# Performance work log

Measured on AMD Instinct MI355X. Metric: run time of the kernel, lower is better.

## Reference

```python
import jax, jax.numpy as jnp
import numpy as np

D_MODEL = 1024
N_HEADS = 16
D_K = D_MODEL // N_HEADS
D_FF = 4096
B, S = 2, 2048
EPS = 1e-5


def setup_inputs() -> dict:
    key = jax.random.key(0)
    ks = jax.random.split(key, 16)
    sc = 0.02
    inp = {
        'x': jax.random.normal(ks[0], (B, S, D_MODEL), dtype=jnp.float32),
        'mask': jnp.ones((B, 1, 1, S), dtype=jnp.int32),
        'Wq': jax.random.normal(ks[1], (D_MODEL, D_MODEL), dtype=jnp.float32) * sc,
        'bq': jnp.zeros((D_MODEL,), dtype=jnp.float32),
        'Wk': jax.random.normal(ks[2], (D_MODEL, D_MODEL), dtype=jnp.float32) * sc,
        'bk': jnp.zeros((D_MODEL,), dtype=jnp.float32),
        'Wv': jax.random.normal(ks[3], (D_MODEL, D_MODEL), dtype=jnp.float32) * sc,
        'bv': jnp.zeros((D_MODEL,), dtype=jnp.float32),
        'Wo': jax.random.normal(ks[4], (D_MODEL, D_MODEL), dtype=jnp.float32) * sc,
        'bo': jnp.zeros((D_MODEL,), dtype=jnp.float32),
        'W1': jax.random.normal(ks[5], (D_MODEL, D_FF), dtype=jnp.float32) * sc,
        'b1': jnp.zeros((D_FF,), dtype=jnp.float32),
        'W2': jax.random.normal(ks[6], (D_FF, D_MODEL), dtype=jnp.float32) * sc,
        'b2': jnp.zeros((D_MODEL,), dtype=jnp.float32),
        'g1': jnp.ones((D_MODEL,), dtype=jnp.float32),
        'be1': jnp.zeros((D_MODEL,), dtype=jnp.float32),
        'g2': jnp.ones((D_MODEL,), dtype=jnp.float32),
        'be2': jnp.zeros((D_MODEL,), dtype=jnp.float32),
    }
    return inp


def _layernorm(x, g, b):
    mu = jnp.mean(x, axis=-1, keepdims=True)
    var = jnp.mean(jnp.square(x - mu), axis=-1, keepdims=True)
    return (x - mu) * jax.lax.rsqrt(var + EPS) * g + b


def _split_heads(x):
    b, s, _ = x.shape
    return x.reshape(b, s, N_HEADS, D_K).transpose(0, 2, 1, 3)  # [B,H,S,Dk]


def reference(x, mask, Wq, bq, Wk, bk, Wv, bv, Wo, bo, W1, b1, W2, b2, g1, be1, g2, be2):
    Q = _split_heads(x @ Wq + bq)
    K = _split_heads(x @ Wk + bk)
    V = _split_heads(x @ Wv + bv)
    scores = jnp.einsum('bhqd,bhkd->bhqk', Q, K) / jnp.sqrt(jnp.float32(D_K))
    scores = jnp.where(mask == 0, -jnp.inf, scores)
    attn = jax.nn.softmax(scores, axis=-1)
    ctx = jnp.einsum('bhqk,bhkd->bhqd', attn, V)
    ctx = ctx.transpose(0, 2, 1, 3).reshape(x.shape[0], x.shape[1], D_MODEL)
    attn_out = ctx @ Wo + bo
    h = _layernorm(x + attn_out, g1, be1)
    ff = jax.nn.relu(h @ W1 + b1) @ W2 + b2
    return _layernorm(h + ff, g2, be2)
```

## Files before the change

kernel.cpp:

```cpp
#include <hip/hip_runtime.h>
#include <hip/hip_bf16.h>

#define D_MODELC 1024
#define D_FFC    4096
#define N_HEADSC 16
#define BATCHC   2
#define SEQC     2048
#define M_TOK    (BATCHC*SEQC)

typedef __attribute__((ext_vector_type(4)))  float f32x4;
typedef __attribute__((ext_vector_type(16))) float f32x16;
typedef __attribute__((ext_vector_type(8)))  short s16x8;
using bf16_t = __hip_bfloat16;

static __device__ __forceinline__ unsigned short f2bf_u16(float f) {
  bf16_t h = __float2bfloat16(f);
  return __builtin_bit_cast(unsigned short, h);
}

static __device__ __forceinline__ unsigned int cvt_pk_bf16(float lo, float hi2) {
  unsigned int r;
  asm("v_cvt_pk_bf16_f32 %0, %1, %2" : "=v"(r) : "v"(lo), "v"(hi2));
  return r;
}

#define ASYNC_COPY16(dst_lds, src_g) \
  __builtin_amdgcn_global_load_lds((const __attribute__((address_space(1))) void*)(src_g), \
                                   (__attribute__((address_space(3))) void*)(dst_lds), 16, 0, 0)

__global__ __launch_bounds__(256) void k_transpose_f32_bf16(
    const float* __restrict__ in, bf16_t* __restrict__ out, int R, int C) {
  __shared__ float tile[32][33];
  int tx = threadIdx.x & 31, ty = threadIdx.x >> 5;
  int c0 = blockIdx.x * 32, r0 = blockIdx.y * 32;
#pragma unroll
  for (int i = 0; i < 4; ++i)
    tile[ty + i * 8][tx] = in[(size_t)(r0 + ty + i * 8) * C + c0 + tx];
  __syncthreads();
#pragma unroll
  for (int i = 0; i < 4; ++i)
    out[(size_t)(c0 + ty + i * 8) * R + r0 + tx] = __float2bfloat16(tile[tx][ty + i * 8]);
}

__global__ __launch_bounds__(256) void k_f32_to_bf16(
    const float* __restrict__ in, bf16_t* __restrict__ out, int n4) {
  int i = blockIdx.x * 256 + threadIdx.x;
  if (i < n4) {
    float4 v = ((const float4*)in)[i];
    short4 o;
    o.x = (short)f2bf_u16(v.x);
    o.y = (short)f2bf_u16(v.y);
    o.z = (short)f2bf_u16(v.z);
    o.w = (short)f2bf_u16(v.w);
    ((short4*)out)[i] = o;
  }
}

__global__ __launch_bounds__(256) void k_pack_bias(
    const float* __restrict__ bq, const float* __restrict__ bk,
    const float* __restrict__ bv, float* __restrict__ out) {
  int i = blockIdx.x * 256 + threadIdx.x;
  float v = (i < 1024) ? bq[i] : (i < 2048) ? bk[i - 1024] : bv[i - 2048];
  out[i] = v;
}

#define GBK 64

__global__ __launch_bounds__(256, 2) void k_gemm(
    const bf16_t* __restrict__ A, const bf16_t* __restrict__ BT,
    const float* __restrict__ bias,
    float* __restrict__ p0, float* __restrict__ p1,
    void* __restrict__ Cout, int M, int N, int K,
    int lda, int ldb, int ldc, int mode, int nsplit) {
  __shared__ __align__(16) bf16_t Asm[128 * GBK];
  __shared__ __align__(16) bf16_t Bsm[128 * GBK];

  const int nbn = N / 128;
  const int nwg = gridDim.x;
  const int cpx = nwg >> 3;
  int wg = (blockIdx.x & 7) * cpx + (blockIdx.x >> 3);
  int kslice = 0;
  if (nsplit == 2) { kslice = wg & 1; wg >>= 1; }
  const int mb = wg / nbn, nb = wg % nbn;
  const int row0 = mb * 128, col0 = nb * 128;
  A  += (size_t)kslice * K;
  BT += (size_t)kslice * K;

  const int tid = threadIdx.x;
  const int w = tid >> 6, lane = tid & 63;
  const int lr = lane & 15, lg = lane >> 4;
  const int wr = w >> 1, wc = w & 1;
  const int wbase = tid & 192;

  f32x4 acc[4][4];
#pragma unroll
  for (int m = 0; m < 4; ++m)
#pragma unroll
    for (int n = 0; n < 4; ++n) acc[m][n] = (f32x4){0.f, 0.f, 0.f, 0.f};

  for (int k0 = 0; k0 < K; k0 += GBK) {
    __syncthreads();
#pragma unroll
    for (int i = 0; i < 4; ++i) {
      int c = i * 256 + tid;
      int row = c >> 3;
      int sg = (c & 7) ^ (row & 7);
      ASYNC_COPY16(Asm + (size_t)(i * 256 + wbase) * 8,
                   A + (size_t)(row0 + row) * lda + k0 + sg * 8);
    }
#pragma unroll
    for (int i = 0; i < 4; ++i) {
      int c = i * 256 + tid;
      int row = c >> 3;
      int sg = (c & 7) ^ (row & 7);
      ASYNC_COPY16(Bsm + (size_t)(i * 256 + wbase) * 8,
                   BT + (size_t)(col0 + row) * ldb + k0 + sg * 8);
    }
    __syncthreads();
#pragma unroll
    for (int kst = 0; kst < 2; ++kst) {
      const int sl = ((kst * 4 + lg) ^ (lr & 7)) * 8;
      s16x8 af[4], bfr[4];
#pragma unroll
      for (int m = 0; m < 4; ++m)
        af[m] = *(const s16x8*)(Asm + (size_t)(wr * 64 + m * 16 + lr) * GBK + sl);
#pragma unroll
      for (int n = 0; n < 4; ++n)
        bfr[n] = *(const s16x8*)(Bsm + (size_t)(wc * 64 + n * 16 + lr) * GBK + sl);
#pragma unroll
      for (int m = 0; m < 4; ++m)
#pragma unroll
        for (int n = 0; n < 4; ++n)
          acc[m][n] = __builtin_amdgcn_mfma_f32_16x16x32_bf16(af[m], bfr[n], acc[m][n], 0, 0, 0);
    }
  }

  float* outf = (kslice == 0) ? p0 : p1;
  bf16_t* outh = (bf16_t*)Cout;
#pragma unroll
  for (int m = 0; m < 4; ++m) {
    int grow = row0 + wr * 64 + m * 16 + lg * 4;
#pragma unroll
    for (int n = 0; n < 4; ++n) {
      int gcol = col0 + wc * 64 + n * 16 + lr;
      float bv = (mode == 4) ? 0.f : bias[gcol];
      float cs = (mode == 3 && gcol < 1024) ? 0.18033688f : 1.f;
#pragma unroll
      for (int r = 0; r < 4; ++r) {
        float v = (acc[m][n][r] + bv) * cs;
        size_t idx = (size_t)(grow + r) * ldc + gcol;
        if (mode == 4) {
          outf[idx] = v;
        } else {
          if (mode == 1) v = fmaxf(v, 0.f);
          outh[idx] = __float2bfloat16(v);
        }
      }
    }
  }
}

__global__ __launch_bounds__(256, 2) void k_attn(
    const bf16_t* __restrict__ qkv, const int* __restrict__ mask,
    bf16_t* __restrict__ ctx) {
  const int bid = blockIdx.x;
  const int qt = bid & 15;
  const int h  = (bid >> 4) & 15;
  const int b  = bid >> 8;
  const int tid = threadIdx.x;
  const int w = tid >> 6, lane = tid & 63;
  const int l31 = lane & 31, hi = lane >> 5;

  __shared__ __align__(16) bf16_t Kl[2][64][64];
  __shared__ __align__(16) bf16_t VT[2][64][72];
  __shared__ __align__(16) float  mskf[2][64];

  const int tokb = b * SEQC;
  const int q0 = qt * 128 + w * 32;

  s16x8 qfrag[4];
  {
    const bf16_t* qp = qkv + (size_t)(tokb + q0 + l31) * 3072 + h * 64 + hi * 8;
#pragma unroll
    for (int s = 0; s < 4; ++s) qfrag[s] = *(const s16x8*)(qp + s * 16);
  }

  char* klc = (char*)&Kl[0][0][0];
  char* vtc = (char*)&VT[0][0][0];

  s16x8 vr[2];
  float mreg = 1.f;

#define STAGE_K(buf, kb)                                                              \
  {                                                                                   \
    _Pragma("unroll")                                                                 \
    for (int ii = 0; ii < 2; ++ii) {                                                  \
      int chunk = w * 2 + ii;                                                         \
      int row = chunk * 8 + (lane >> 3);                                              \
      int seg = (lane & 7) ^ (row & 7);                                               \
      const bf16_t* src = qkv + (size_t)(tokb + (kb) + row) * 3072 + 1024 + h * 64 + seg * 8; \
      ASYNC_COPY16(&Kl[buf][chunk * 8][0], src);                                      \
    }                                                                                 \
  }

#define LOAD_V(kb)                                                                    \
  {                                                                                   \
    _Pragma("unroll")                                                                 \
    for (int i = 0; i < 2; ++i) {                                                     \
      int c = tid + i * 256;                                                          \
      int key = c & 63, d0 = (c >> 6) * 8;                                            \
      vr[i] = *(const s16x8*)(qkv + (size_t)(tokb + (kb) + key) * 3072 + 2048 + h * 64 + d0); \
    }                                                                                 \
  }

#define WRITE_V(buf)                                                                  \
  {                                                                                   \
    _Pragma("unroll")                                                                 \
    for (int i = 0; i < 2; ++i) {                                                     \
      int c = tid + i * 256;                                                          \
      int key = c & 63, d0 = (c >> 6) * 8;                                            \
      const bf16_t* e = (const bf16_t*)&vr[i];                                        \
      _Pragma("unroll")                                                               \
      for (int j = 0; j < 8; ++j) {                                                   \
        int d = d0 + j;                                                               \
        *(bf16_t*)(vtc + (buf) * 9216 + d * 144 + (key >> 3) * 16 + (key & 7) * 2) = e[j]; \
      }                                                                               \
    }                                                                                 \
  }

  STAGE_K(0, 0)
  LOAD_V(0)
  if (tid < 64) mreg = mask[tokb + tid] ? 1.f : 0.f;
  WRITE_V(0)
  if (tid < 64) mskf[0][tid] = mreg;

  f32x16 o[2];
#pragma unroll
  for (int d = 0; d < 2; ++d)
#pragma unroll
    for (int i = 0; i < 16; ++i) o[d][i] = 0.f;
  float psum = 0.f;

  __syncthreads();

  for (int kt = 0; kt < SEQC / 64; ++kt) {
    const int kb = kt * 64;
    const int cur = kt & 1, nxt = cur ^ 1;
    const bool more = (kt < SEQC / 64 - 1);

    if (more) {
      STAGE_K(nxt, kb + 64)
      LOAD_V(kb + 64)
      if (tid < 64) mreg = mask[tokb + kb + 64 + tid] ? 1.f : 0.f;
    }

    f32x16 st[2];
#pragma unroll
    for (int kk = 0; kk < 2; ++kk)
#pragma unroll
      for (int i = 0; i < 16; ++i) st[kk][i] = 0.f;
#pragma unroll
    for (int step = 0; step < 4; ++step) {
#pragma unroll
      for (int kb2 = 0; kb2 < 2; ++kb2) {
        int key = kb2 * 32 + l31;
        int seg = (2 * step + hi) ^ (lane & 7);
        s16x8 kf = *(const s16x8*)(klc + cur * 8192 + key * 128 + seg * 16);
        st[kb2] = __builtin_amdgcn_mfma_f32_32x32x16_bf16(kf, qfrag[step], st[kb2], 0, 0, 0);
      }
    }

    s16x8 pf[4];
#pragma unroll
    for (int kb2 = 0; kb2 < 2; ++kb2) {
      float pa[16];
#pragma unroll
      for (int g = 0; g < 4; ++g) {
        f32x4 mm = *(const f32x4*)((char*)&mskf[cur][0] + (kb2 * 128 + g * 32 + hi * 16));
#pragma unroll
        for (int rr = 0; rr < 4; ++rr) {
          float e = __builtin_exp2f(st[kb2][g * 4 + rr]) * mm[rr];
          pa[g * 4 + rr] = e;
          psum += e;
        }
      }
      unsigned int wv[8];
#pragma unroll
      for (int u = 0; u < 8; ++u) wv[u] = cvt_pk_bf16(pa[2 * u], pa[2 * u + 1]);
      unsigned int x1 = hi ? wv[0] : wv[2]; x1 = (unsigned int)__shfl_xor((int)x1, 32);
      unsigned int x2 = hi ? wv[1] : wv[3]; x2 = (unsigned int)__shfl_xor((int)x2, 32);
      unsigned int x3 = hi ? wv[4] : wv[6]; x3 = (unsigned int)__shfl_xor((int)x3, 32);
      unsigned int x4 = hi ? wv[5] : wv[7]; x4 = (unsigned int)__shfl_xor((int)x4, 32);
      unsigned int f0[4], f1[4];
      f0[0] = hi ? x1 : wv[0];  f0[1] = hi ? x2 : wv[1];
      f0[2] = hi ? wv[2] : x1;  f0[3] = hi ? wv[3] : x2;
      f1[0] = hi ? x3 : wv[4];  f1[1] = hi ? x4 : wv[5];
      f1[2] = hi ? wv[6] : x3;  f1[3] = hi ? wv[7] : x4;
      pf[kb2 * 2 + 0] = __builtin_bit_cast(s16x8, *(ulong2*)f0);
      pf[kb2 * 2 + 1] = __builtin_bit_cast(s16x8, *(ulong2*)f1);
    }

#pragma unroll
    for (int ks = 0; ks < 4; ++ks) {
#pragma unroll
      for (int dblk = 0; dblk < 2; ++dblk) {
        int d = dblk * 32 + l31;
        s16x8 vf = *(const s16x8*)(vtc + cur * 9216 + d * 144 + (2 * ks + hi) * 16);
        o[dblk] = __builtin_amdgcn_mfma_f32_32x32x16_bf16(pf[ks], vf, o[dblk], 0, 0, 0);
      }
    }

    if (more) {
      WRITE_V(nxt)
      if (tid < 64) mskf[nxt][tid] = mreg;
    }

    __syncthreads();
  }

  psum += __shfl_xor(psum, 32);
  float rs[16];
#pragma unroll
  for (int r = 0; r < 16; ++r) {
    int qq = (r & 3) + 8 * (r >> 2) + 4 * hi;
    rs[r] = __shfl(psum, qq);
  }
#pragma unroll
  for (int dblk = 0; dblk < 2; ++dblk)
#pragma unroll
    for (int r = 0; r < 16; ++r) {
      int qq = (r & 3) + 8 * (r >> 2) + 4 * hi;
      int tok = tokb + q0 + qq;
      ctx[(size_t)tok * 1024 + h * 64 + dblk * 32 + l31] = __float2bfloat16(o[dblk][r] / rs[r]);
    }
#undef STAGE_K
#undef LOAD_V
#undef WRITE_V
}

__global__ __launch_bounds__(256) void k_ln_res2(
    const float* __restrict__ p0, const float* __restrict__ p1,
    const float* __restrict__ res, const float* __restrict__ bias,
    const float* __restrict__ g, const float* __restrict__ be,
    float* __restrict__ outf, bf16_t* __restrict__ outh) {
  const int row = blockIdx.x, tid = threadIdx.x;
  const size_t base = (size_t)row * D_MODELC;
  const float4 a  = ((const float4*)(p0 + base))[tid];
  const float4 bq = ((const float4*)(p1 + base))[tid];
  const float4 c  = ((const float4*)(res + base))[tid];
  const float4 bi = ((const float4*)bias)[tid];
  float4 v;
  v.x = a.x + bq.x + c.x + bi.x;
  v.y = a.y + bq.y + c.y + bi.y;
  v.z = a.z + bq.z + c.z + bi.z;
  v.w = a.w + bq.w + c.w + bi.w;
  float s1 = v.x + v.y + v.z + v.w;
  float s2 = v.x * v.x + v.y * v.y + v.z * v.z + v.w * v.w;
#pragma unroll
  for (int mm = 1; mm < 64; mm <<= 1) {
    s1 += __shfl_xor(s1, mm);
    s2 += __shfl_xor(s2, mm);
  }
  __shared__ float sa[4], sb[4];
  const int wv = tid >> 6;
  if ((tid & 63) == 0) { sa[wv] = s1; sb[wv] = s2; }
  __syncthreads();
  s1 = sa[0] + sa[1] + sa[2] + sa[3];
  s2 = sb[0] + sb[1] + sb[2] + sb[3];
  const float mu = s1 * (1.f / D_MODELC);
  const float var = s2 * (1.f / D_MODELC) - mu * mu;
  const float rsq = rsqrtf(var + 1e-5f);
  const float4 gg = ((const float4*)g)[tid];
  const float4 bb = ((const float4*)be)[tid];
  float4 oo;
  oo.x = (v.x - mu) * rsq * gg.x + bb.x;
  oo.y = (v.y - mu) * rsq * gg.y + bb.y;
  oo.z = (v.z - mu) * rsq * gg.z + bb.z;
  oo.w = (v.w - mu) * rsq * gg.w + bb.w;
  ((float4*)(outf + base))[tid] = oo;
  if (outh) {
    short4 ob;
    ob.x = (short)f2bf_u16(oo.x);
    ob.y = (short)f2bf_u16(oo.y);
    ob.z = (short)f2bf_u16(oo.z);
    ob.w = (short)f2bf_u16(oo.w);
    ((short4*)(outh + base))[tid] = ob;
  }
}

extern "C" void kernel_launch(void* const* d_in, const int* in_sizes, int n_in,
                              void* d_out, int out_size, void* d_ws, size_t ws_size,
                              hipStream_t stream) {
  (void)in_sizes; (void)n_in; (void)out_size; (void)ws_size;
  const float* x   = (const float*)d_in[0];
  const int* mask  = (const int*)d_in[1];
  const float* Wq  = (const float*)d_in[2];
  const float* bq  = (const float*)d_in[3];
  const float* Wk  = (const float*)d_in[4];
  const float* bk  = (const float*)d_in[5];
  const float* Wv  = (const float*)d_in[6];
  const float* bv  = (const float*)d_in[7];
  const float* Wo  = (const float*)d_in[8];
  const float* bo  = (const float*)d_in[9];
  const float* W1  = (const float*)d_in[10];
  const float* b1  = (const float*)d_in[11];
  const float* W2  = (const float*)d_in[12];
  const float* b2  = (const float*)d_in[13];
  const float* g1  = (const float*)d_in[14];
  const float* be1 = (const float*)d_in[15];
  const float* g2  = (const float*)d_in[16];
  const float* be2 = (const float*)d_in[17];

  char* ws = (char*)d_ws;
  const size_t D = D_MODELC, F = D_FFC, M = M_TOK;
  const size_t SZ_X16  = M * D * 2;
  const size_t SZ_QKV  = M * 3 * D * 2;
  bf16_t* x16   = (bf16_t*)ws;
  bf16_t* ff1   = (bf16_t*)ws;
  bf16_t* qkvb  = (bf16_t*)(ws + SZ_X16);
  size_t off = SZ_X16 + SZ_QKV;
  bf16_t* ctx   = (bf16_t*)(ws + off); off += M * D * 2;
  bf16_t* wqkvT = (bf16_t*)(ws + off); off += 3 * D * D * 2;
  bf16_t* woT   = (bf16_t*)(ws + off); off += D * D * 2;
  bf16_t* w1T   = (bf16_t*)(ws + off); off += D * F * 2;
  bf16_t* w2T   = (bf16_t*)(ws + off); off += D * F * 2;
  float*  partA = (float*)(ws + off);  off += M * D * 4;
  float*  hbuf  = (float*)(ws + off);  off += M * D * 4;
  bf16_t* h16   = (bf16_t*)(ws + off); off += M * D * 2;
  float*  partB = (float*)(ws + off);  off += M * D * 4;
  float*  bqkv  = (float*)(ws + off);  off += 3 * D * 4;

  k_transpose_f32_bf16<<<dim3(32, 32), 256, 0, stream>>>(Wq, wqkvT, 1024, 1024);
  k_transpose_f32_bf16<<<dim3(32, 32), 256, 0, stream>>>(Wk, wqkvT + 1024 * 1024, 1024, 1024);
  k_transpose_f32_bf16<<<dim3(32, 32), 256, 0, stream>>>(Wv, wqkvT + 2 * 1024 * 1024, 1024, 1024);
  k_transpose_f32_bf16<<<dim3(32, 32), 256, 0, stream>>>(Wo, woT, 1024, 1024);
  k_transpose_f32_bf16<<<dim3(128, 32), 256, 0, stream>>>(W1, w1T, 1024, 4096);
  k_transpose_f32_bf16<<<dim3(32, 128), 256, 0, stream>>>(W2, w2T, 4096, 1024);
  k_f32_to_bf16<<<4096, 256, 0, stream>>>(x, x16, (int)(M * D / 4));
  k_pack_bias<<<12, 256, 0, stream>>>(bq, bk, bv, bqkv);

  k_gemm<<<768, 256, 0, stream>>>(x16, wqkvT, bqkv, nullptr, nullptr, qkvb,
                                  4096, 3072, 1024, 1024, 1024, 3072, 3, 1);

  k_attn<<<BATCHC * N_HEADSC * (SEQC / 128), 256, 0, stream>>>(qkvb, mask, ctx);

  k_gemm<<<512, 256, 0, stream>>>(ctx, woT, nullptr, partA, partB, nullptr,
                                  4096, 1024, 512, 1024, 1024, 1024, 4, 2);
  k_ln_res2<<<4096, 256, 0, stream>>>(partA, partB, x, bo, g1, be1, hbuf, h16);

  k_gemm<<<1024, 256, 0, stream>>>(h16, w1T, b1, nullptr, nullptr, ff1,
                                   4096, 4096, 1024, 1024, 1024, 4096, 1, 1);
  k_gemm<<<512, 256, 0, stream>>>(ff1, w2T, nullptr, partA, partB, nullptr,
                                  4096, 1024, 2048, 4096, 4096, 1024, 4, 2);
  k_ln_res2<<<4096, 256, 0, stream>>>(partA, partB, hbuf, b2, g2, be2, (float*)d_out, nullptr);
}
```

Measured before the change: 275.2 us.

## Stage V via async LDS copy and transpose-read it, add all-valid mask fast path

Replaces the register-load-then-scalar-transposed-write of V tiles with direct async global-to-LDS copies in a permuted layout. V fragments are then read with the ds_read_b64_tr_b16 transpose-load instruction. The cross-half P fragment exchange now uses v_permlane32_swap instead of shfl_xor plus selects. A per-tile all-valid mask flag is computed with a ballot so the exp loop can skip the mask multiply. The intent is to cut LDS store traffic, VGPR pressure and VALU work in the attention loop, at the cost of relying on gfx950-specific instructions and a hand-placed waitcnt.

```diff
diff --git a/kernel.cpp b/kernel.cpp
--- a/kernel.cpp
+++ b/kernel.cpp
@@ -23,6 +23,8 @@
   asm("v_cvt_pk_bf16_f32 %0, %1, %2" : "=v"(r) : "v"(lo), "v"(hi2));
   return r;
 }
+
+#define PSWAP(a, b) asm volatile("v_permlane32_swap_b32 %0, %1" : "+v"(a), "+v"(b))
 
 #define ASYNC_COPY16(dst_lds, src_g) \
   __builtin_amdgcn_global_load_lds((const __attribute__((address_space(1))) void*)(src_g), \
@@ -170,10 +172,11 @@
   const int tid = threadIdx.x;
   const int w = tid >> 6, lane = tid & 63;
   const int l31 = lane & 31, hi = lane >> 5;
+  const int wbase = tid & 192;
 
   __shared__ __align__(16) bf16_t Kl[2][64][64];
-  __shared__ __align__(16) bf16_t VT[2][64][72];
-  __shared__ __align__(16) float  mskf[2][64];
+  __shared__ __align__(16) bf16_t Vl[2][4096];
+  __shared__ __align__(16) float  mskf[2][68];
 
   const int tokb = b * SEQC;
   const int q0 = qt * 128 + w * 32;
@@ -186,9 +189,10 @@
   }
 
   char* klc = (char*)&Kl[0][0][0];
-  char* vtc = (char*)&VT[0][0][0];
-
-  s16x8 vr[2];
+  bf16_t* Vl0 = &Vl[0][0];
+  const unsigned vbase =
+      (unsigned)(size_t)(__attribute__((address_space(3))) bf16_t*)Vl0 + lane * 8;
+
   float mreg = 1.f;
 
 #define STAGE_K(buf, kb)                                                              \
@@ -203,36 +207,34 @@
     }                                                                                 \
   }
 
-#define LOAD_V(kb)                                                                    \
+#define STAGE_V(buf, kb)                                                              \
   {                                                                                   \
     _Pragma("unroll")                                                                 \
-    for (int i = 0; i < 2; ++i) {                                                     \
-      int c = tid + i * 256;                                                          \
-      int key = c & 63, d0 = (c >> 6) * 8;                                            \
-      vr[i] = *(const s16x8*)(qkv + (size_t)(tokb + (kb) + key) * 3072 + 2048 + h * 64 + d0); \
+    for (int ii = 0; ii < 2; ++ii) {                                                  \
+      const int c = tid + ii * 256;                                                   \
+      const int L = c >> 3;                                                           \
+      const int vf_ = L >> 4, vt_ = (L >> 3) & 1, vdb_ = (L >> 2) & 1;                \
+      const int vh_ = (L >> 1) & 1, vdo_ = L & 1;                                     \
+      const int vkey = 16 * vf_ + 8 * vh_ + 4 * vt_ + ((c & 7) >> 1);                 \
+      const int vd = ((vdb_ * 2 + vdo_) << 4) + (c & 1) * 8;                          \
+      const bf16_t* vsrc = qkv + (size_t)(tokb + (kb) + vkey) * 3072 + 2048 + h * 64 + vd; \
+      ASYNC_COPY16(Vl0 + (size_t)(buf) * 4096 + (size_t)(ii * 256 + wbase) * 8, vsrc); \
     }                                                                                 \
   }
 
-#define WRITE_V(buf)                                                                  \
+#define STAGE_M(buf, kb)                                                              \
   {                                                                                   \
-    _Pragma("unroll")                                                                 \
-    for (int i = 0; i < 2; ++i) {                                                     \
-      int c = tid + i * 256;                                                          \
-      int key = c & 63, d0 = (c >> 6) * 8;                                            \
-      const bf16_t* e = (const bf16_t*)&vr[i];                                        \
-      _Pragma("unroll")                                                               \
-      for (int j = 0; j < 8; ++j) {                                                   \
-        int d = d0 + j;                                                               \
-        *(bf16_t*)(vtc + (buf) * 9216 + d * 144 + (key >> 3) * 16 + (key & 7) * 2) = e[j]; \
-      }                                                                               \
+    if (w == 0) {                                                                     \
+      mreg = mask[tokb + (kb) + lane] ? 1.f : 0.f;                                    \
+      mskf[buf][lane] = mreg;                                                         \
+      unsigned long long z = __ballot(mreg == 0.f);                                   \
+      if (lane == 0) mskf[buf][64] = (z == 0ull) ? 1.f : 0.f;                         \
     }                                                                                 \
   }
 
   STAGE_K(0, 0)
-  LOAD_V(0)
-  if (tid < 64) mreg = mask[tokb + tid] ? 1.f : 0.f;
-  WRITE_V(0)
-  if (tid < 64) mskf[0][tid] = mreg;
+  STAGE_V(0, 0)
+  STAGE_M(0, 0)
 
   f32x16 o[2];
 #pragma unroll
@@ -250,8 +252,8 @@
 
     if (more) {
       STAGE_K(nxt, kb + 64)
-      LOAD_V(kb + 64)
-      if (tid < 64) mreg = mask[tokb + kb + 64 + tid] ? 1.f : 0.f;
+      STAGE_V(nxt, kb + 64)
+      STAGE_M(nxt, kb + 64)
     }
 
     f32x16 st[2];
@@ -270,50 +272,64 @@
       }
     }
 
+    const unsigned va = vbase + cur * 8192;
+    ulong tr[4][2][2];
+#pragma unroll
+    for (int f = 0; f < 4; ++f)
+#pragma unroll
+      for (int db = 0; db < 2; ++db)
+        asm volatile("ds_read_b64_tr_b16 %0, %2 offset:%c3\n\t"
+                     "ds_read_b64_tr_b16 %1, %2 offset:%c4"
+                     : "=v"(tr[f][db][0]), "=v"(tr[f][db][1])
+                     : "v"(va), "i"((f * 16 + db * 4) * 128), "i"((f * 16 + 8 + db * 4) * 128));
+
+    const bool allv = (mskf[cur][64] != 0.f);
     s16x8 pf[4];
 #pragma unroll
     for (int kb2 = 0; kb2 < 2; ++kb2) {
       float pa[16];
-#pragma unroll
-      for (int g = 0; g < 4; ++g) {
-        f32x4 mm = *(const f32x4*)((char*)&mskf[cur][0] + (kb2 * 128 + g * 32 + hi * 16));
-#pragma unroll
-        for (int rr = 0; rr < 4; ++rr) {
-          float e = __builtin_exp2f(st[kb2][g * 4 + rr]) * mm[rr];
-          pa[g * 4 + rr] = e;
+      if (allv) {
+#pragma unroll
+        for (int i = 0; i < 16; ++i) {
+          float e = __builtin_exp2f(st[kb2][i]);
+          pa[i] = e;
           psum += e;
+        }
+      } else {
+#pragma unroll
+        for (int g = 0; g < 4; ++g) {
+          f32x4 mm = *(const f32x4*)((char*)&mskf[cur][0] + (kb2 * 128 + g * 32 + hi * 16));
+#pragma unroll
+          for (int rr = 0; rr < 4; ++rr) {
+            float e = __builtin_exp2f(st[kb2][g * 4 + rr]) * mm[rr];
+            pa[g * 4 + rr] = e;
+            psum += e;
+          }
         }
       }
       unsigned int wv[8];
 #pragma unroll
       for (int u = 0; u < 8; ++u) wv[u] = cvt_pk_bf16(pa[2 * u], pa[2 * u + 1]);
-      unsigned int x1 = hi ? wv[0] : wv[2]; x1 = (unsigned int)__shfl_xor((int)x1, 32);
-      unsigned int x2 = hi ? wv[1] : wv[3]; x2 = (unsigned int)__shfl_xor((int)x2, 32);
-      unsigned int x3 = hi ? wv[4] : wv[6]; x3 = (unsigned int)__shfl_xor((int)x3, 32);
-      unsigned int x4 = hi ? wv[5] : wv[7]; x4 = (unsigned int)__shfl_xor((int)x4, 32);
-      unsigned int f0[4], f1[4];
-      f0[0] = hi ? x1 : wv[0];  f0[1] = hi ? x2 : wv[1];
-      f0[2] = hi ? wv[2] : x1;  f0[3] = hi ? wv[3] : x2;
-      f1[0] = hi ? x3 : wv[4];  f1[1] = hi ? x4 : wv[5];
-      f1[2] = hi ? wv[6] : x3;  f1[3] = hi ? wv[7] : x4;
-      pf[kb2 * 2 + 0] = __builtin_bit_cast(s16x8, *(ulong2*)f0);
-      pf[kb2 * 2 + 1] = __builtin_bit_cast(s16x8, *(ulong2*)f1);
-    }
-
-#pragma unroll
-    for (int ks = 0; ks < 4; ++ks) {
-#pragma unroll
-      for (int dblk = 0; dblk < 2; ++dblk) {
-        int d = dblk * 32 + l31;
-        s16x8 vf = *(const s16x8*)(vtc + cur * 9216 + d * 144 + (2 * ks + hi) * 16);
-        o[dblk] = __builtin_amdgcn_mfma_f32_32x32x16_bf16(pf[ks], vf, o[dblk], 0, 0, 0);
+      unsigned int a0 = wv[0], b0 = wv[2]; PSWAP(a0, b0);
+      unsigned int a1 = wv[1], b1 = wv[3]; PSWAP(a1, b1);
+      unsigned int a2 = wv[4], b2 = wv[6]; PSWAP(a2, b2);
+      unsigned int a3 = wv[5], b3 = wv[7]; PSWAP(a3, b3);
+      uint4 u0 = {a0, a1, b0, b1};
+      uint4 u1 = {a2, a3, b2, b3};
+      pf[kb2 * 2 + 0] = __builtin_bit_cast(s16x8, u0);
+      pf[kb2 * 2 + 1] = __builtin_bit_cast(s16x8, u1);
+    }
+
+    asm volatile("s_waitcnt lgkmcnt(0)" ::: "memory");
+    __builtin_amdgcn_sched_barrier(0);
+#pragma unroll
+    for (int f = 0; f < 4; ++f)
+#pragma unroll
+      for (int db = 0; db < 2; ++db) {
+        ulong2 uv = {tr[f][db][0], tr[f][db][1]};
+        s16x8 vfr = __builtin_bit_cast(s16x8, uv);
+        o[db] = __builtin_amdgcn_mfma_f32_32x32x16_bf16(pf[f], vfr, o[db], 0, 0, 0);
       }
-    }
-
-    if (more) {
-      WRITE_V(nxt)
-      if (tid < 64) mskf[nxt][tid] = mreg;
-    }
 
     __syncthreads();
   }
@@ -334,8 +350,8 @@
       ctx[(size_t)tok * 1024 + h * 64 + dblk * 32 + l31] = __float2bfloat16(o[dblk][r] / rs[r]);
     }
 #undef STAGE_K
-#undef LOAD_V
-#undef WRITE_V
+#undef STAGE_V
+#undef STAGE_M
 }
 
 __global__ __launch_bounds__(256) void k_ln_res2(
```

Result: faster. 268.9 us (-2.3%).
